# Kernel optimization log

Hardware: AMD Instinct MI355X
Metric: run time of the kernel (lower is better)

## Reference

```python
import jax, jax.numpy as jnp
import numpy as np

N = 100000   # nodes
E = 1600000  # edges
FEAT = 128
HID = 128
TGT = 64
L = 3
G = 512      # graphs in batch


def setup_inputs() -> dict:
    key = jax.random.key(0)
    ks = jax.random.split(key, 16)
    s = 0.05
    return {
        "x": jax.random.normal(ks[0], (N, FEAT), jnp.float32),
        "edge_index": jax.random.randint(ks[1], (2, E), 0, N, dtype=jnp.int32),
        "batch": jnp.sort(jax.random.randint(ks[2], (N,), 0, G, dtype=jnp.int32)),
        "conv_w1": jax.random.normal(ks[3], (L, FEAT, HID), jnp.float32) * s,
        "conv_b1": jax.random.normal(ks[4], (L, HID), jnp.float32) * s,
        "conv_w2": jax.random.normal(ks[5], (L, HID, HID), jnp.float32) * s,
        "conv_b2": jax.random.normal(ks[6], (L, HID), jnp.float32) * s,
        "eps": jnp.zeros((L,), jnp.float32),
        "gn_scale": jnp.ones((L, HID), jnp.float32),
        "gn_weight": jnp.ones((L, HID), jnp.float32),
        "gn_bias": jnp.zeros((L, HID), jnp.float32),
        "proj_w1": jax.random.normal(ks[7], (L, HID, HID), jnp.float32) * s,
        "proj_b1": jax.random.normal(ks[8], (L, HID), jnp.float32) * s,
        "proj_w2": jax.random.normal(ks[9], (L, HID, TGT), jnp.float32) * s,
        "proj_b2": jax.random.normal(ks[10], (L, TGT), jnp.float32) * s,
    }


def _graph_norm(h, batch, counts, scale, weight, bias):
    # per-graph mean -> scatter back to nodes
    mean = jax.ops.segment_sum(h, batch, num_segments=G) / counts
    sub = h - mean[batch] * scale
    var = jax.ops.segment_sum(sub * sub, batch, num_segments=G) / counts
    std = jnp.sqrt(var + 1e-8)
    return weight * sub / std[batch] + bias


def reference(x, edge_index, batch, conv_w1, conv_b1, conv_w2, conv_b2, eps,
              gn_scale, gn_weight, gn_bias, proj_w1, proj_b1, proj_w2, proj_b2):
    src, dst = edge_index[0], edge_index[1]
    counts = jnp.maximum(
        jax.ops.segment_sum(jnp.ones((N, 1), x.dtype), batch, num_segments=G), 1.0)
    h = x
    z_cat = []
    for l in range(L):
        # GINConv: aggr_j->i then 2-layer MLP
        aggr = jax.ops.segment_sum(h[src], dst, num_segments=N)
        h = (1.0 + eps[l]) * h + aggr
        h = jax.nn.relu(h @ conv_w1[l] + conv_b1[l]) @ conv_w2[l] + conv_b2[l]
        # GraphNorm
        h = _graph_norm(h, batch, counts, gn_scale[l], gn_weight[l], gn_bias[l])
        h = jax.nn.relu(h)
        # projection MLP + global add pool
        z = jax.nn.relu(h @ proj_w1[l] + proj_b1[l]) @ proj_w2[l] + proj_b2[l]
        z_cat.append(jax.ops.segment_sum(z, batch, num_segments=G))
    return jnp.concatenate(z_cat, axis=-1)  # [G, L*TGT]
```

## Files before the change

kernel.cpp:

```cpp
#include <hip/hip_runtime.h>

#define NN 100000
#define EE 1600000
#define HIDD 128
#define TGTT 64
#define GGG 512
#define NBK 98
#define CAPB 17408
#define ABLK 200

typedef unsigned short ushort_t;
typedef __attribute__((ext_vector_type(8))) short short8;
typedef __attribute__((ext_vector_type(4))) float f32x4;
typedef __attribute__((ext_vector_type(4))) unsigned short us4;

__device__ __forceinline__ float b2f(ushort_t u) {
    union { unsigned int i; float f; } v; v.i = ((unsigned int)u) << 16; return v.f;
}
__device__ __forceinline__ ushort_t f2b(float f) {
    union { float f; unsigned int i; } v; v.f = f;
    unsigned int r = (v.i + 0x7fffu + ((v.i >> 16) & 1u)) >> 16;
    return (ushort_t)r;
}

__global__ void k_goff(const int* __restrict__ batch, int* __restrict__ goff) {
    int t = blockIdx.x * blockDim.x + threadIdx.x;
    if (t > GGG) return;
    int lo = 0, hi = NN;
    while (lo < hi) { int mid = (lo + hi) >> 1; if (batch[mid] < t) lo = mid + 1; else hi = mid; }
    goff[t] = lo;
}

__global__ __launch_bounds__(256) void k_cvt(const float* __restrict__ x, ushort_t* __restrict__ Xb) {
    long i = (long)blockIdx.x * 256 + threadIdx.x;
    if (i >= (long)NN * 32) return;
    float4 v = ((const float4*)x)[i];
    us4 o; o.x = f2b(v.x); o.y = f2b(v.y); o.z = f2b(v.z); o.w = f2b(v.w);
    ((us4*)Xb)[i] = o;
}

__global__ __launch_bounds__(256) void k_prep(const float* __restrict__ cw1, const float* __restrict__ cw2,
                                              const float* __restrict__ pw1, ushort_t* __restrict__ Wt) {
    __shared__ ushort_t sW[128 * 129];
    int mat = blockIdx.x;
    int l = mat / 3, j = mat % 3;
    const float* src = (j == 0 ? cw1 : j == 1 ? cw2 : pw1) + (size_t)l * HIDD * HIDD;
    ushort_t* dst = Wt + (size_t)mat * HIDD * HIDD;
    for (int i = threadIdx.x; i < HIDD * HIDD; i += 256) {
        int k = i >> 7, n = i & 127;
        sW[n * 129 + k] = f2b(src[i]);
    }
    __syncthreads();
    for (int i = threadIdx.x; i < HIDD * HIDD; i += 256) {
        dst[i] = sW[(i >> 7) * 129 + (i & 127)];
    }
}

__global__ __launch_bounds__(256) void k_binA(const int* __restrict__ ei,
                                              int* __restrict__ gcnt,
                                              unsigned int* __restrict__ bbuf) {
    __shared__ int cnt[NBK], base[NBK], cur[NBK];
    int t = threadIdx.x;
    if (t < NBK) cnt[t] = 0;
    __syncthreads();
    int e0 = blockIdx.x * 8000;
    int e1 = min(e0 + 8000, EE);
    for (int e = e0 + t; e < e1; e += 256)
        atomicAdd(&cnt[ei[EE + e] >> 10], 1);
    __syncthreads();
    if (t < NBK) { base[t] = atomicAdd(&gcnt[t], cnt[t]); cur[t] = 0; }
    __syncthreads();
    for (int e = e0 + t; e < e1; e += 256) {
        int s = ei[e], d = ei[EE + e];
        int b = d >> 10;
        int off = base[b] + atomicAdd(&cur[b], 1);
        if (off < CAPB)
            bbuf[(long)b * CAPB + off] = (unsigned int)s | (((unsigned int)d & 1023u) << 17);
    }
}

__global__ void k_bbase(const int* __restrict__ gcnt, int* __restrict__ gbase,
                        int* __restrict__ rowptr) {
    __shared__ int sd[128];
    int t = threadIdx.x;
    int v = (t < NBK) ? gcnt[t] : 0;
    sd[t] = v;
    __syncthreads();
    for (int off = 1; off < 128; off <<= 1) {
        int u = (t >= off) ? sd[t - off] : 0;
        __syncthreads();
        sd[t] += u;
        __syncthreads();
    }
    if (t < NBK) gbase[t] = sd[t] - v;
    if (t == 0) rowptr[NN] = EE;
}

__global__ __launch_bounds__(256) void k_csr(const int* __restrict__ gcnt,
                                             const int* __restrict__ gbase,
                                             const unsigned int* __restrict__ bbuf,
                                             int* __restrict__ rowptr, int* __restrict__ csr) {
    __shared__ int ldeg[1024], lcur[1024], tsum[256];
    int b = blockIdx.x, t = threadIdx.x;
    int cnt = min(gcnt[b], CAPB);
    int base = gbase[b];
    const unsigned int* bb = bbuf + (long)b * CAPB;
#pragma unroll
    for (int i = 0; i < 4; i++) ldeg[t + 256 * i] = 0;
    __syncthreads();
    for (int i = t; i < cnt; i += 256) atomicAdd(&ldeg[bb[i] >> 17], 1);
    __syncthreads();
    int d0 = ldeg[4 * t], d1 = ldeg[4 * t + 1], d2 = ldeg[4 * t + 2], d3 = ldeg[4 * t + 3];
    int tot = d0 + d1 + d2 + d3;
    tsum[t] = tot;
    __syncthreads();
    for (int off = 1; off < 256; off <<= 1) {
        int u = (t >= off) ? tsum[t - off] : 0;
        __syncthreads();
        tsum[t] += u;
        __syncthreads();
    }
    int texcl = tsum[t] - tot;
    int p0 = base + texcl, p1 = p0 + d0, p2 = p1 + d1, p3 = p2 + d2;
    lcur[4 * t] = p0; lcur[4 * t + 1] = p1; lcur[4 * t + 2] = p2; lcur[4 * t + 3] = p3;
    int gnode = b * 1024 + 4 * t;
    if (gnode < NN)     rowptr[gnode]     = p0;
    if (gnode + 1 < NN) rowptr[gnode + 1] = p1;
    if (gnode + 2 < NN) rowptr[gnode + 2] = p2;
    if (gnode + 3 < NN) rowptr[gnode + 3] = p3;
    __syncthreads();
    for (int i = t; i < cnt; i += 256) {
        unsigned int en = bb[i];
        int pos = atomicAdd(&lcur[en >> 17], 1);
        csr[pos] = (int)(en & 0x1FFFFu);
    }
}

__global__ __launch_bounds__(256) void k_gather(const ushort_t* __restrict__ hin,
                                                const int* __restrict__ rowptr,
                                                const int* __restrict__ csr,
                                                const float* __restrict__ eps, int l,
                                                ushort_t* __restrict__ A) {
    int node = blockIdx.x * 16 + (threadIdx.x >> 4);
    if (node >= NN) return;
    int lane = threadIdx.x & 15;
    int off = lane << 3;
    float e1 = 1.0f + eps[l];
    short8 h = *(const short8*)(hin + ((long)node << 7) + off);
    float acc[8];
#pragma unroll
    for (int t = 0; t < 8; t++) acc[t] = e1 * b2f((ushort_t)h[t]);
    int jb = rowptr[node], je = rowptr[node + 1];
    int j = jb;
    for (; j + 8 <= je; j += 8) {
        int s0 = csr[j], s1 = csr[j + 1], s2 = csr[j + 2], s3 = csr[j + 3];
        int s4 = csr[j + 4], s5 = csr[j + 5], s6 = csr[j + 6], s7 = csr[j + 7];
        short8 v0 = *(const short8*)(hin + ((long)s0 << 7) + off);
        short8 v1 = *(const short8*)(hin + ((long)s1 << 7) + off);
        short8 v2 = *(const short8*)(hin + ((long)s2 << 7) + off);
        short8 v3 = *(const short8*)(hin + ((long)s3 << 7) + off);
        short8 v4 = *(const short8*)(hin + ((long)s4 << 7) + off);
        short8 v5 = *(const short8*)(hin + ((long)s5 << 7) + off);
        short8 v6 = *(const short8*)(hin + ((long)s6 << 7) + off);
        short8 v7 = *(const short8*)(hin + ((long)s7 << 7) + off);
#pragma unroll
        for (int t = 0; t < 8; t++)
            acc[t] += ((b2f((ushort_t)v0[t]) + b2f((ushort_t)v1[t])) +
                       (b2f((ushort_t)v2[t]) + b2f((ushort_t)v3[t]))) +
                      ((b2f((ushort_t)v4[t]) + b2f((ushort_t)v5[t])) +
                       (b2f((ushort_t)v6[t]) + b2f((ushort_t)v7[t])));
    }
    for (; j + 4 <= je; j += 4) {
        int s0 = csr[j], s1 = csr[j + 1], s2 = csr[j + 2], s3 = csr[j + 3];
        short8 v0 = *(const short8*)(hin + ((long)s0 << 7) + off);
        short8 v1 = *(const short8*)(hin + ((long)s1 << 7) + off);
        short8 v2 = *(const short8*)(hin + ((long)s2 << 7) + off);
        short8 v3 = *(const short8*)(hin + ((long)s3 << 7) + off);
#pragma unroll
        for (int t = 0; t < 8; t++)
            acc[t] += (b2f((ushort_t)v0[t]) + b2f((ushort_t)v1[t])) +
                      (b2f((ushort_t)v2[t]) + b2f((ushort_t)v3[t]));
    }
    for (; j < je; j++) {
        int s = csr[j];
        short8 v = *(const short8*)(hin + ((long)s << 7) + off);
#pragma unroll
        for (int t = 0; t < 8; t++) acc[t] += b2f((ushort_t)v[t]);
    }
    short8 o;
#pragma unroll
    for (int t = 0; t < 8; t++) o[t] = (short)f2b(acc[t]);
    *(short8*)(A + ((long)node << 7) + off) = o;
}

#define LSTR 136
__global__ __launch_bounds__(256) void k_mlp2(const ushort_t* __restrict__ X,
                                              const ushort_t* __restrict__ Wt1, const float* __restrict__ B1,
                                              const ushort_t* __restrict__ Wt2, const float* __restrict__ B2,
                                              ushort_t* __restrict__ Y) {
    __shared__ ushort_t sX[128 * LSTR];
    int tid = threadIdx.x;
    long base = (long)blockIdx.x * 128;
#pragma unroll
    for (int c = 0; c < 8; c++) {
        int idx = c * 256 + tid;
        int row = idx >> 4, cw = idx & 15;
        long grow = base + row;
        short8 v = (short8)0;
        if (grow < NN) v = *(const short8*)(X + (grow << 7) + (cw << 3));
        *(short8*)(sX + row * LSTR + (cw << 3)) = v;
    }
    __syncthreads();

    int w = tid >> 6, lane = tid & 63, q = lane >> 4, l16 = lane & 15;
    int r0 = w * 16, r1 = 64 + w * 16;

    short8 a0[4], a1[4];
#pragma unroll
    for (int c = 0; c < 4; c++) {
        a0[c] = *(const short8*)(sX + (r0 + l16) * LSTR + q * 8 + c * 32);
        a1[c] = *(const short8*)(sX + (r1 + l16) * LSTR + q * 8 + c * 32);
    }

    f32x4 acc0[8], acc1[8];
#pragma unroll
    for (int nt = 0; nt < 8; nt++) {
        int col = nt * 16 + l16;
        float bias = B1[col];
        f32x4 c0 = {bias, bias, bias, bias};
        f32x4 c1 = c0;
        const ushort_t* bB = Wt1 + col * HIDD + q * 8;
#pragma unroll
        for (int c = 0; c < 4; c++) {
            short8 b = *(const short8*)(bB + c * 32);
            c0 = __builtin_amdgcn_mfma_f32_16x16x32_bf16(a0[c], b, c0, 0, 0, 0);
            c1 = __builtin_amdgcn_mfma_f32_16x16x32_bf16(a1[c], b, c1, 0, 0, 0);
        }
        acc0[nt] = c0; acc1[nt] = c1;
    }
    __syncthreads();

#pragma unroll
    for (int nt = 0; nt < 8; nt++) {
        int col = nt * 16 + l16;
#pragma unroll
        for (int r = 0; r < 4; r++) {
            sX[(r0 + q * 4 + r) * LSTR + col] = f2b(fmaxf(acc0[nt][r], 0.f));
            sX[(r1 + q * 4 + r) * LSTR + col] = f2b(fmaxf(acc1[nt][r], 0.f));
        }
    }
    __syncthreads();

#pragma unroll
    for (int c = 0; c < 4; c++) {
        a0[c] = *(const short8*)(sX + (r0 + l16) * LSTR + q * 8 + c * 32);
        a1[c] = *(const short8*)(sX + (r1 + l16) * LSTR + q * 8 + c * 32);
    }
#pragma unroll
    for (int nt = 0; nt < 8; nt++) {
        int col = nt * 16 + l16;
        float bias = B2[col];
        f32x4 c0 = {bias, bias, bias, bias};
        f32x4 c1 = c0;
        const ushort_t* bB = Wt2 + col * HIDD + q * 8;
#pragma unroll
        for (int c = 0; c < 4; c++) {
            short8 b = *(const short8*)(bB + c * 32);
            c0 = __builtin_amdgcn_mfma_f32_16x16x32_bf16(a0[c], b, c0, 0, 0, 0);
            c1 = __builtin_amdgcn_mfma_f32_16x16x32_bf16(a1[c], b, c1, 0, 0, 0);
        }
#pragma unroll
        for (int r = 0; r < 4; r++) {
            long row0 = base + r0 + q * 4 + r;
            long row1 = base + r1 + q * 4 + r;
            if (row0 < NN) Y[(row0 << 7) + col] = f2b(c0[r]);
            if (row1 < NN) Y[(row1 << 7) + col] = f2b(c1[r]);
        }
    }
}

__global__ __launch_bounds__(512) void k_gstat(const ushort_t* __restrict__ Hraw,
                                               const int* __restrict__ goff,
                                               const float* __restrict__ scale,
                                               const float* __restrict__ weight,
                                               float* __restrict__ msb, float* __restrict__ invb) {
    int g = blockIdx.x;
    int s = goff[g], e = goff[g + 1];
    float cnt = (float)max(e - s, 1);
    int fp = threadIdx.x & 63;
    int r = threadIdx.x >> 6;
    int f0 = fp * 2;
    float s0 = 0.f, s1 = 0.f, q0 = 0.f, q1 = 0.f;
    for (int i = s + r; i < e; i += 8) {
        unsigned int v = *(const unsigned int*)(Hraw + ((long)i << 7) + f0);
        float a = b2f((ushort_t)(v & 0xffffu));
        float b = b2f((ushort_t)(v >> 16));
        s0 += a; q0 += a * a; s1 += b; q1 += b * b;
    }
    __shared__ float red[4][8][64];
    red[0][r][fp] = s0; red[1][r][fp] = q0; red[2][r][fp] = s1; red[3][r][fp] = q1;
    __syncthreads();
    if (r == 0) {
#pragma unroll
        for (int k = 1; k < 8; k++) {
            s0 += red[0][k][fp]; q0 += red[1][k][fp];
            s1 += red[2][k][fp]; q1 += red[3][k][fp];
        }
        float mean0 = s0 / cnt, mean1 = s1 / cnt;
        float ms0 = mean0 * scale[f0], ms1 = mean1 * scale[f0 + 1];
        float var0 = q0 / cnt - 2.f * ms0 * mean0 + ms0 * ms0;
        float var1 = q1 / cnt - 2.f * ms1 * mean1 + ms1 * ms1;
        msb[g * HIDD + f0] = ms0;
        msb[g * HIDD + f0 + 1] = ms1;
        invb[g * HIDD + f0] = weight[f0] / sqrtf(var0 + 1e-8f);
        invb[g * HIDD + f0 + 1] = weight[f0 + 1] / sqrtf(var1 + 1e-8f);
    }
}

__global__ __launch_bounds__(256) void k_proj(const ushort_t* __restrict__ Hraw,
                                              const int* __restrict__ batch,
                                              const float* __restrict__ msb, const float* __restrict__ invb,
                                              const float* __restrict__ gnb,
                                              const ushort_t* __restrict__ Wt, const float* __restrict__ B,
                                              ushort_t* __restrict__ Hn, ushort_t* __restrict__ Z) {
    __shared__ ushort_t sX[128 * LSTR];
    int tid = threadIdx.x;
    long base = (long)blockIdx.x * 128;
#pragma unroll
    for (int c = 0; c < 8; c++) {
        int idx = c * 256 + tid;
        int row = idx >> 4, cw = idx & 15;
        long grow = base + row;
        short8 v = (short8)0;
        if (grow < NN) {
            short8 raw = *(const short8*)(Hraw + (grow << 7) + (cw << 3));
            int g = batch[grow];
            const float* msp = msb + g * HIDD + (cw << 3);
            const float* ivp = invb + g * HIDD + (cw << 3);
            const float* gbp = gnb + (cw << 3);
            float4 m0 = *(const float4*)msp, m1 = *(const float4*)(msp + 4);
            float4 i0 = *(const float4*)ivp, i1 = *(const float4*)(ivp + 4);
            float4 g0 = *(const float4*)gbp, g1 = *(const float4*)(gbp + 4);
            float mv[8] = {m0.x, m0.y, m0.z, m0.w, m1.x, m1.y, m1.z, m1.w};
            float iv[8] = {i0.x, i0.y, i0.z, i0.w, i1.x, i1.y, i1.z, i1.w};
            float gv[8] = {g0.x, g0.y, g0.z, g0.w, g1.x, g1.y, g1.z, g1.w};
#pragma unroll
            for (int t = 0; t < 8; t++) {
                float val = (b2f((ushort_t)raw[t]) - mv[t]) * iv[t] + gv[t];
                v[t] = (short)f2b(val > 0.f ? val : 0.f);
            }
            *(short8*)(Hn + (grow << 7) + (cw << 3)) = v;
        }
        *(short8*)(sX + row * LSTR + (cw << 3)) = v;
    }
    __syncthreads();

    int w = tid >> 6, lane = tid & 63, q = lane >> 4, l16 = lane & 15;
    int r0 = w * 16, r1 = 64 + w * 16;
    short8 a0[4], a1[4];
#pragma unroll
    for (int c = 0; c < 4; c++) {
        a0[c] = *(const short8*)(sX + (r0 + l16) * LSTR + q * 8 + c * 32);
        a1[c] = *(const short8*)(sX + (r1 + l16) * LSTR + q * 8 + c * 32);
    }
#pragma unroll
    for (int nt = 0; nt < 8; nt++) {
        int col = nt * 16 + l16;
        float bias = B[col];
        f32x4 c0 = {bias, bias, bias, bias};
        f32x4 c1 = c0;
        const ushort_t* bB = Wt + col * HIDD + q * 8;
#pragma unroll
        for (int c = 0; c < 4; c++) {
            short8 b = *(const short8*)(bB + c * 32);
            c0 = __builtin_amdgcn_mfma_f32_16x16x32_bf16(a0[c], b, c0, 0, 0, 0);
            c1 = __builtin_amdgcn_mfma_f32_16x16x32_bf16(a1[c], b, c1, 0, 0, 0);
        }
#pragma unroll
        for (int r = 0; r < 4; r++) {
            long row0 = base + r0 + q * 4 + r;
            long row1 = base + r1 + q * 4 + r;
            if (row0 < NN) Z[(row0 << 7) + col] = f2b(fmaxf(c0[r], 0.f));
            if (row1 < NN) Z[(row1 << 7) + col] = f2b(fmaxf(c1[r], 0.f));
        }
    }
}

__global__ __launch_bounds__(512) void k_poolout(const ushort_t* __restrict__ Z, const int* __restrict__ goff,
                                                 const float* __restrict__ W, const float* __restrict__ B,
                                                 float* __restrict__ out, int l) {
    int g = blockIdx.x;
    int s = goff[g], e = goff[g + 1];
    int f = threadIdx.x & 127;
    int r = threadIdx.x >> 7;
    float sum = 0.f;
    for (int i = s + r; i < e; i += 4) sum += b2f(Z[(long)i * HIDD + f]);
    __shared__ float red[4][128];
    red[r][f] = sum;
    __syncthreads();
    __shared__ float p[128];
    if (r == 0) p[f] = red[0][f] + red[1][f] + red[2][f] + red[3][f];
    __syncthreads();
    int t = threadIdx.x;
    if (t < TGTT) {
        float cnt = (float)(e - s);
        float acc = cnt * B[t];
        for (int k = 0; k < HIDD; k++) acc += p[k] * W[k * TGTT + t];
        out[(long)g * (3 * TGTT) + l * TGTT + t] = acc;
    }
}

extern "C" void kernel_launch(void* const* d_in, const int* in_sizes, int n_in,
                              void* d_out, int out_size, void* d_ws, size_t ws_size,
                              hipStream_t stream) {
    const float* x    = (const float*)d_in[0];
    const int*   ei   = (const int*)d_in[1];
    const int*   batch= (const int*)d_in[2];
    const float* cw1  = (const float*)d_in[3];
    const float* cb1  = (const float*)d_in[4];
    const float* cw2  = (const float*)d_in[5];
    const float* cb2  = (const float*)d_in[6];
    const float* eps  = (const float*)d_in[7];
    const float* gsc  = (const float*)d_in[8];
    const float* gw   = (const float*)d_in[9];
    const float* gb   = (const float*)d_in[10];
    const float* pw1  = (const float*)d_in[11];
    const float* pb1  = (const float*)d_in[12];
    const float* pw2  = (const float*)d_in[13];
    const float* pb2  = (const float*)d_in[14];
    float* out = (float*)d_out;

    ushort_t* Xb   = (ushort_t*)d_ws;
    ushort_t* Hn   = Xb;
    ushort_t* A    = Xb + (size_t)NN * HIDD;
    ushort_t* Hraw = A + (size_t)NN * HIDD;
    ushort_t* Wt   = Hraw + (size_t)NN * HIDD;
    float* msb     = (float*)(Wt + (size_t)9 * HIDD * HIDD);
    float* invb    = msb + (size_t)GGG * HIDD;
    int* goff   = (int*)(invb + (size_t)GGG * HIDD);
    int* rowptr = goff + (GGG + 1);
    int* gcnt   = rowptr + (NN + 1);
    int* gbase  = gcnt + NBK;
    int* csr    = gbase + NBK;
    unsigned int* bbuf = (unsigned int*)(csr + EE);

    k_goff<<<3, 256, 0, stream>>>(batch, goff);
    k_cvt<<<(int)(((long)NN * 32 + 255) / 256), 256, 0, stream>>>(x, Xb);
    k_prep<<<9, 256, 0, stream>>>(cw1, cw2, pw1, Wt);

    hipMemsetAsync(gcnt, 0, NBK * sizeof(int), stream);
    k_binA<<<ABLK, 256, 0, stream>>>(ei, gcnt, bbuf);
    k_bbase<<<1, 128, 0, stream>>>(gcnt, gbase, rowptr);
    k_csr<<<NBK, 256, 0, stream>>>(gcnt, gbase, bbuf, rowptr, csr);

    for (int l = 0; l < 3; l++) {
        const ushort_t* hin = (l == 0) ? Xb : Hn;
        ushort_t* Wt1 = Wt + (size_t)(l * 3 + 0) * HIDD * HIDD;
        ushort_t* Wt2 = Wt + (size_t)(l * 3 + 1) * HIDD * HIDD;
        ushort_t* Wtp = Wt + (size_t)(l * 3 + 2) * HIDD * HIDD;
        k_gather<<<(NN + 15) / 16, 256, 0, stream>>>(hin, rowptr, csr, eps, l, A);
        k_mlp2<<<(NN + 127) / 128, 256, 0, stream>>>(A, Wt1, cb1 + l * HIDD, Wt2, cb2 + l * HIDD, Hraw);
        k_gstat<<<GGG, 512, 0, stream>>>(Hraw, goff, gsc + l * HIDD, gw + l * HIDD, msb, invb);
        k_proj<<<(NN + 127) / 128, 256, 0, stream>>>(Hraw, batch, msb, invb, gb + l * HIDD,
                                                     Wtp, pb1 + l * HIDD, Hn, A);
        k_poolout<<<GGG, 512, 0, stream>>>(A, goff, pw2 + (size_t)l * HIDD * TGTT, pb2 + l * TGTT, out, l);
    }
}
```

Baseline: 685.6 us.

## Fuse neighbor gather into MLP kernel and fuse pooling into projection kernel

The CSR neighbor aggregation now runs inside the MLP kernel and writes directly to shared memory, so the aggregated activations no longer make a round trip through global memory. The projection kernel now also segment-sums its ReLU output per graph in shared memory and adds the result into a small pooled buffer with atomics. A tiny per-graph kernel then applies the final linear layer. This removes two full-size intermediate writes and reads per layer, but the fused gather kernel has fewer blocks to hide gather latency, and the float atomics make the sum order nondeterministic.

```diff
diff --git a/kernel.cpp b/kernel.cpp
--- a/kernel.cpp
+++ b/kernel.cpp
@@ -8,6 +8,7 @@
 #define NBK 98
 #define CAPB 17408
 #define ABLK 200
+#define LSTR 136
 
 typedef unsigned short ushort_t;
 typedef __attribute__((ext_vector_type(8))) short short8;
@@ -136,92 +137,82 @@
     }
 }
 
-__global__ __launch_bounds__(256) void k_gather(const ushort_t* __restrict__ hin,
-                                                const int* __restrict__ rowptr,
-                                                const int* __restrict__ csr,
-                                                const float* __restrict__ eps, int l,
-                                                ushort_t* __restrict__ A) {
-    int node = blockIdx.x * 16 + (threadIdx.x >> 4);
-    if (node >= NN) return;
-    int lane = threadIdx.x & 15;
-    int off = lane << 3;
-    float e1 = 1.0f + eps[l];
-    short8 h = *(const short8*)(hin + ((long)node << 7) + off);
-    float acc[8];
-#pragma unroll
-    for (int t = 0; t < 8; t++) acc[t] = e1 * b2f((ushort_t)h[t]);
-    int jb = rowptr[node], je = rowptr[node + 1];
-    int j = jb;
-    for (; j + 8 <= je; j += 8) {
-        int s0 = csr[j], s1 = csr[j + 1], s2 = csr[j + 2], s3 = csr[j + 3];
-        int s4 = csr[j + 4], s5 = csr[j + 5], s6 = csr[j + 6], s7 = csr[j + 7];
-        short8 v0 = *(const short8*)(hin + ((long)s0 << 7) + off);
-        short8 v1 = *(const short8*)(hin + ((long)s1 << 7) + off);
-        short8 v2 = *(const short8*)(hin + ((long)s2 << 7) + off);
-        short8 v3 = *(const short8*)(hin + ((long)s3 << 7) + off);
-        short8 v4 = *(const short8*)(hin + ((long)s4 << 7) + off);
-        short8 v5 = *(const short8*)(hin + ((long)s5 << 7) + off);
-        short8 v6 = *(const short8*)(hin + ((long)s6 << 7) + off);
-        short8 v7 = *(const short8*)(hin + ((long)s7 << 7) + off);
-#pragma unroll
-        for (int t = 0; t < 8; t++)
-            acc[t] += ((b2f((ushort_t)v0[t]) + b2f((ushort_t)v1[t])) +
-                       (b2f((ushort_t)v2[t]) + b2f((ushort_t)v3[t]))) +
-                      ((b2f((ushort_t)v4[t]) + b2f((ushort_t)v5[t])) +
-                       (b2f((ushort_t)v6[t]) + b2f((ushort_t)v7[t])));
-    }
-    for (; j + 4 <= je; j += 4) {
-        int s0 = csr[j], s1 = csr[j + 1], s2 = csr[j + 2], s3 = csr[j + 3];
-        short8 v0 = *(const short8*)(hin + ((long)s0 << 7) + off);
-        short8 v1 = *(const short8*)(hin + ((long)s1 << 7) + off);
-        short8 v2 = *(const short8*)(hin + ((long)s2 << 7) + off);
-        short8 v3 = *(const short8*)(hin + ((long)s3 << 7) + off);
-#pragma unroll
-        for (int t = 0; t < 8; t++)
-            acc[t] += (b2f((ushort_t)v0[t]) + b2f((ushort_t)v1[t])) +
-                      (b2f((ushort_t)v2[t]) + b2f((ushort_t)v3[t]));
-    }
-    for (; j < je; j++) {
-        int s = csr[j];
-        short8 v = *(const short8*)(hin + ((long)s << 7) + off);
-#pragma unroll
-        for (int t = 0; t < 8; t++) acc[t] += b2f((ushort_t)v[t]);
-    }
-    short8 o;
-#pragma unroll
-    for (int t = 0; t < 8; t++) o[t] = (short)f2b(acc[t]);
-    *(short8*)(A + ((long)node << 7) + off) = o;
-}
-
-#define LSTR 136
-__global__ __launch_bounds__(256) void k_mlp2(const ushort_t* __restrict__ X,
+__global__ __launch_bounds__(256) void k_gmlp(const ushort_t* __restrict__ hin,
+                                              const int* __restrict__ rowptr,
+                                              const int* __restrict__ csr,
+                                              const float* __restrict__ eps, int l,
                                               const ushort_t* __restrict__ Wt1, const float* __restrict__ B1,
                                               const ushort_t* __restrict__ Wt2, const float* __restrict__ B2,
                                               ushort_t* __restrict__ Y) {
     __shared__ ushort_t sX[128 * LSTR];
     int tid = threadIdx.x;
     long base = (long)blockIdx.x * 128;
-#pragma unroll
-    for (int c = 0; c < 8; c++) {
-        int idx = c * 256 + tid;
-        int row = idx >> 4, cw = idx & 15;
-        long grow = base + row;
-        short8 v = (short8)0;
-        if (grow < NN) v = *(const short8*)(X + (grow << 7) + (cw << 3));
-        *(short8*)(sX + row * LSTR + (cw << 3)) = v;
-    }
-    __syncthreads();
-
-    int w = tid >> 6, lane = tid & 63, q = lane >> 4, l16 = lane & 15;
+    int lane = tid & 15, ng = tid >> 4;
+    int off = lane << 3;
+    float e1 = 1.0f + eps[l];
+
+#pragma unroll 1
+    for (int it = 0; it < 8; it++) {
+        int row = it * 16 + ng;
+        long node = base + row;
+        short8 o = (short8)0;
+        if (node < NN) {
+            short8 h = *(const short8*)(hin + (node << 7) + off);
+            float acc[8];
+#pragma unroll
+            for (int t = 0; t < 8; t++) acc[t] = e1 * b2f((ushort_t)h[t]);
+            int jb = rowptr[node], je = rowptr[node + 1];
+            int j = jb;
+            for (; j + 8 <= je; j += 8) {
+                int s0 = csr[j], s1 = csr[j + 1], s2 = csr[j + 2], s3 = csr[j + 3];
+                int s4 = csr[j + 4], s5 = csr[j + 5], s6 = csr[j + 6], s7 = csr[j + 7];
+                short8 v0 = *(const short8*)(hin + ((long)s0 << 7) + off);
+                short8 v1 = *(const short8*)(hin + ((long)s1 << 7) + off);
+                short8 v2 = *(const short8*)(hin + ((long)s2 << 7) + off);
+                short8 v3 = *(const short8*)(hin + ((long)s3 << 7) + off);
+                short8 v4 = *(const short8*)(hin + ((long)s4 << 7) + off);
+                short8 v5 = *(const short8*)(hin + ((long)s5 << 7) + off);
+                short8 v6 = *(const short8*)(hin + ((long)s6 << 7) + off);
+                short8 v7 = *(const short8*)(hin + ((long)s7 << 7) + off);
+#pragma unroll
+                for (int t = 0; t < 8; t++)
+                    acc[t] += ((b2f((ushort_t)v0[t]) + b2f((ushort_t)v1[t])) +
+                               (b2f((ushort_t)v2[t]) + b2f((ushort_t)v3[t]))) +
+                              ((b2f((ushort_t)v4[t]) + b2f((ushort_t)v5[t])) +
+                               (b2f((ushort_t)v6[t]) + b2f((ushort_t)v7[t])));
+            }
+            for (; j + 4 <= je; j += 4) {
+                int s0 = csr[j], s1 = csr[j + 1], s2 = csr[j + 2], s3 = csr[j + 3];
+                short8 v0 = *(const short8*)(hin + ((long)s0 << 7) + off);
+                short8 v1 = *(const short8*)(hin + ((long)s1 << 7) + off);
+                short8 v2 = *(const short8*)(hin + ((long)s2 << 7) + off);
+                short8 v3 = *(const short8*)(hin + ((long)s3 << 7) + off);
+#pragma unroll
+                for (int t = 0; t < 8; t++)
+                    acc[t] += (b2f((ushort_t)v0[t]) + b2f((ushort_t)v1[t])) +
+                              (b2f((ushort_t)v2[t]) + b2f((ushort_t)v3[t]));
+            }
+            for (; j < je; j++) {
+                int s = csr[j];
+                short8 v = *(const short8*)(hin + ((long)s << 7) + off);
+#pragma unroll
+                for (int t = 0; t < 8; t++) acc[t] += b2f((ushort_t)v[t]);
+            }
+#pragma unroll
+            for (int t = 0; t < 8; t++) o[t] = (short)f2b(acc[t]);
+        }
+        *(short8*)(sX + row * LSTR + off) = o;
+    }
+    __syncthreads();
+
+    int w = tid >> 6, l64 = tid & 63, q = l64 >> 4, l16 = l64 & 15;
     int r0 = w * 16, r1 = 64 + w * 16;
-
     short8 a0[4], a1[4];
 #pragma unroll
     for (int c = 0; c < 4; c++) {
         a0[c] = *(const short8*)(sX + (r0 + l16) * LSTR + q * 8 + c * 32);
         a1[c] = *(const short8*)(sX + (r1 + l16) * LSTR + q * 8 + c * 32);
     }
-
     f32x4 acc0[8], acc1[8];
 #pragma unroll
     for (int nt = 0; nt < 8; nt++) {
@@ -239,7 +230,6 @@
         acc0[nt] = c0; acc1[nt] = c1;
     }
     __syncthreads();
-
 #pragma unroll
     for (int nt = 0; nt < 8; nt++) {
         int col = nt * 16 + l16;
@@ -250,7 +240,6 @@
         }
     }
     __syncthreads();
-
 #pragma unroll
     for (int c = 0; c < 4; c++) {
         a0[c] = *(const short8*)(sX + (r0 + l16) * LSTR + q * 8 + c * 32);
@@ -283,7 +272,8 @@
                                                const int* __restrict__ goff,
                                                const float* __restrict__ scale,
                                                const float* __restrict__ weight,
-                                               float* __restrict__ msb, float* __restrict__ invb) {
+                                               float* __restrict__ msb, float* __restrict__ invb,
+                                               float* __restrict__ pooled) {
     int g = blockIdx.x;
     int s = goff[g], e = goff[g + 1];
     float cnt = (float)max(e - s, 1);
@@ -314,16 +304,19 @@
         msb[g * HIDD + f0 + 1] = ms1;
         invb[g * HIDD + f0] = weight[f0] / sqrtf(var0 + 1e-8f);
         invb[g * HIDD + f0 + 1] = weight[f0 + 1] / sqrtf(var1 + 1e-8f);
-    }
-}
-
-__global__ __launch_bounds__(256) void k_proj(const ushort_t* __restrict__ Hraw,
-                                              const int* __restrict__ batch,
-                                              const float* __restrict__ msb, const float* __restrict__ invb,
-                                              const float* __restrict__ gnb,
-                                              const ushort_t* __restrict__ Wt, const float* __restrict__ B,
-                                              ushort_t* __restrict__ Hn, ushort_t* __restrict__ Z) {
+        pooled[g * HIDD + f0] = 0.f;
+        pooled[g * HIDD + f0 + 1] = 0.f;
+    }
+}
+
+__global__ __launch_bounds__(256) void k_projpool(const ushort_t* __restrict__ Hraw,
+                                                  const int* __restrict__ batch,
+                                                  const float* __restrict__ msb, const float* __restrict__ invb,
+                                                  const float* __restrict__ gnb,
+                                                  const ushort_t* __restrict__ Wt, const float* __restrict__ B,
+                                                  ushort_t* __restrict__ Hn, float* __restrict__ pooled) {
     __shared__ ushort_t sX[128 * LSTR];
+    __shared__ int sgid[128];
     int tid = threadIdx.x;
     long base = (long)blockIdx.x * 128;
 #pragma unroll
@@ -335,6 +328,7 @@
         if (grow < NN) {
             short8 raw = *(const short8*)(Hraw + (grow << 7) + (cw << 3));
             int g = batch[grow];
+            if (cw == 0) sgid[row] = g;
             const float* msp = msb + g * HIDD + (cw << 3);
             const float* ivp = invb + g * HIDD + (cw << 3);
             const float* gbp = gnb + (cw << 3);
@@ -350,12 +344,14 @@
                 v[t] = (short)f2b(val > 0.f ? val : 0.f);
             }
             *(short8*)(Hn + (grow << 7) + (cw << 3)) = v;
+        } else if (cw == 0) {
+            sgid[row] = -1;
         }
         *(short8*)(sX + row * LSTR + (cw << 3)) = v;
     }
     __syncthreads();
 
-    int w = tid >> 6, lane = tid & 63, q = lane >> 4, l16 = lane & 15;
+    int w = tid >> 6, l64 = tid & 63, q = l64 >> 4, l16 = l64 & 15;
     int r0 = w * 16, r1 = 64 + w * 16;
     short8 a0[4], a1[4];
 #pragma unroll
@@ -363,6 +359,7 @@
         a0[c] = *(const short8*)(sX + (r0 + l16) * LSTR + q * 8 + c * 32);
         a1[c] = *(const short8*)(sX + (r1 + l16) * LSTR + q * 8 + c * 32);
     }
+    f32x4 acc0[8], acc1[8];
 #pragma unroll
     for (int nt = 0; nt < 8; nt++) {
         int col = nt * 16 + l16;
@@ -376,38 +373,48 @@
             c0 = __builtin_amdgcn_mfma_f32_16x16x32_bf16(a0[c], b, c0, 0, 0, 0);
             c1 = __builtin_amdgcn_mfma_f32_16x16x32_bf16(a1[c], b, c1, 0, 0, 0);
         }
+        acc0[nt] = c0; acc1[nt] = c1;
+    }
+    __syncthreads();
+#pragma unroll
+    for (int nt = 0; nt < 8; nt++) {
+        int col = nt * 16 + l16;
 #pragma unroll
         for (int r = 0; r < 4; r++) {
-            long row0 = base + r0 + q * 4 + r;
-            long row1 = base + r1 + q * 4 + r;
-            if (row0 < NN) Z[(row0 << 7) + col] = f2b(fmaxf(c0[r], 0.f));
-            if (row1 < NN) Z[(row1 << 7) + col] = f2b(fmaxf(c1[r], 0.f));
-        }
-    }
-}
-
-__global__ __launch_bounds__(512) void k_poolout(const ushort_t* __restrict__ Z, const int* __restrict__ goff,
-                                                 const float* __restrict__ W, const float* __restrict__ B,
-                                                 float* __restrict__ out, int l) {
+            sX[(r0 + q * 4 + r) * LSTR + col] = f2b(fmaxf(acc0[nt][r], 0.f));
+            sX[(r1 + q * 4 + r) * LSTR + col] = f2b(fmaxf(acc1[nt][r], 0.f));
+        }
+    }
+    __syncthreads();
+
+    int f = tid & 127, half = tid >> 7;
+    int rbeg = half * 64, rend = rbeg + 64;
+    float sum = 0.f;
+    int curg = -1;
+    for (int row = rbeg; row < rend; row++) {
+        int g = sgid[row];
+        if (g != curg) {
+            if (curg >= 0) atomicAdd(&pooled[(long)curg * HIDD + f], sum);
+            sum = 0.f; curg = g;
+        }
+        if (g >= 0) sum += b2f(sX[row * LSTR + f]);
+    }
+    if (curg >= 0) atomicAdd(&pooled[(long)curg * HIDD + f], sum);
+}
+
+__global__ __launch_bounds__(64) void k_out(const float* __restrict__ pooled, const int* __restrict__ goff,
+                                            const float* __restrict__ W, const float* __restrict__ B,
+                                            float* __restrict__ out, int l) {
     int g = blockIdx.x;
-    int s = goff[g], e = goff[g + 1];
-    int f = threadIdx.x & 127;
-    int r = threadIdx.x >> 7;
-    float sum = 0.f;
-    for (int i = s + r; i < e; i += 4) sum += b2f(Z[(long)i * HIDD + f]);
-    __shared__ float red[4][128];
-    red[r][f] = sum;
-    __syncthreads();
+    int t = threadIdx.x;
     __shared__ float p[128];
-    if (r == 0) p[f] = red[0][f] + red[1][f] + red[2][f] + red[3][f];
-    __syncthreads();
-    int t = threadIdx.x;
-    if (t < TGTT) {
-        float cnt = (float)(e - s);
-        float acc = cnt * B[t];
-        for (int k = 0; k < HIDD; k++) acc += p[k] * W[k * TGTT + t];
-        out[(long)g * (3 * TGTT) + l * TGTT + t] = acc;
-    }
+    p[t] = pooled[g * HIDD + t];
+    p[t + 64] = pooled[g * HIDD + 64 + t];
+    __syncthreads();
+    float cnt = (float)(goff[g + 1] - goff[g]);
+    float acc = cnt * B[t];
+    for (int k = 0; k < HIDD; k++) acc += p[k] * W[k * TGTT + t];
+    out[(long)g * (3 * TGTT) + l * TGTT + t] = acc;
 }
 
 extern "C" void kernel_launch(void* const* d_in, const int* in_sizes, int n_in,
@@ -432,12 +439,12 @@
 
     ushort_t* Xb   = (ushort_t*)d_ws;
     ushort_t* Hn   = Xb;
-    ushort_t* A    = Xb + (size_t)NN * HIDD;
-    ushort_t* Hraw = A + (size_t)NN * HIDD;
+    ushort_t* Hraw = Xb + (size_t)NN * HIDD;
     ushort_t* Wt   = Hraw + (size_t)NN * HIDD;
     float* msb     = (float*)(Wt + (size_t)9 * HIDD * HIDD);
     float* invb    = msb + (size_t)GGG * HIDD;
-    int* goff   = (int*)(invb + (size_t)GGG * HIDD);
+    float* pooled  = invb + (size_t)GGG * HIDD;
+    int* goff   = (int*)(pooled + (size_t)GGG * HIDD);
     int* rowptr = goff + (GGG + 1);
     int* gcnt   = rowptr + (NN + 1);
     int* gbase  = gcnt + NBK;
@@ -458,11 +465,11 @@
         ushort_t* Wt1 = Wt + (size_t)(l * 3 + 0) * HIDD * HIDD;
         ushort_t* Wt2 = Wt + (size_t)(l * 3 + 1) * HIDD * HIDD;
         ushort_t* Wtp = Wt + (size_t)(l * 3 + 2) * HIDD * HIDD;
-        k_gather<<<(NN + 15) / 16, 256, 0, stream>>>(hin, rowptr, csr, eps, l, A);
-        k_mlp2<<<(NN + 127) / 128, 256, 0, stream>>>(A, Wt1, cb1 + l * HIDD, Wt2, cb2 + l * HIDD, Hraw);
-        k_gstat<<<GGG, 512, 0, stream>>>(Hraw, goff, gsc + l * HIDD, gw + l * HIDD, msb, invb);
-        k_proj<<<(NN + 127) / 128, 256, 0, stream>>>(Hraw, batch, msb, invb, gb + l * HIDD,
-                                                     Wtp, pb1 + l * HIDD, Hn, A);
-        k_poolout<<<GGG, 512, 0, stream>>>(A, goff, pw2 + (size_t)l * HIDD * TGTT, pb2 + l * TGTT, out, l);
-    }
-}
+        k_gmlp<<<(NN + 127) / 128, 256, 0, stream>>>(hin, rowptr, csr, eps, l,
+                                                     Wt1, cb1 + l * HIDD, Wt2, cb2 + l * HIDD, Hraw);
+        k_gstat<<<GGG, 512, 0, stream>>>(Hraw, goff, gsc + l * HIDD, gw + l * HIDD, msb, invb, pooled);
+        k_projpool<<<(NN + 127) / 128, 256, 0, stream>>>(Hraw, batch, msb, invb, gb + l * HIDD,
+                                                         Wtp, pb1 + l * HIDD, Hn, pooled);
+        k_out<<<GGG, 64, 0, stream>>>(pooled, goff, pw2 + (size_t)l * HIDD * TGTT, pb2 + l * TGTT, out, l);
+    }
+}
```

Measured after the change: 642.2 us. -6.3%, faster.
